# Kernel optimization log

Measured on AMD Instinct MI355X. Metric: run time of the kernel, lower is better.

The kernel has to match this reference:

```python
import jax, jax.numpy as jnp
import numpy as np


def setup_inputs() -> dict:
    key = jax.random.key(0)
    k1, k2 = jax.random.split(key)
    B, H, W, D = 4096, 64, 64, 512
    inputs = jax.random.normal(k1, (B, D), dtype=jnp.float32)
    # keras 'random_uniform' initializer default range [-0.05, 0.05]
    weights_map = jax.random.uniform(k2, (H, W, D), dtype=jnp.float32,
                                     minval=-0.05, maxval=0.05)
    return {"inputs": inputs, "weights_map": weights_map}


def reference(inputs, weights_map):
    # inputs: (B, D); weights_map: (H, W, D)
    H, W, D = weights_map.shape
    flat_w = weights_map.reshape(-1, D)              # (N, D), N = H*W
    # avoids materializing the (B, N, D) difference tensor)
    x_sq = jnp.sum(inputs * inputs, axis=1, keepdims=True)    # (B, 1)
    w_sq = jnp.sum(flat_w * flat_w, axis=1)                   # (N,)
    sq_dist = x_sq - 2.0 * (inputs @ flat_w.T) + w_sq         # (B, N)
    sq_dist = jnp.maximum(sq_dist, 0.0)
    bmu_flat = jnp.argmin(sq_dist, axis=1)                    # (B,)
    bmu_y = (bmu_flat // W).astype(jnp.int32)
    bmu_x = (bmu_flat % W).astype(jnp.int32)
    bmu_indices = jnp.stack([bmu_y, bmu_x], axis=1)           # (B, 2)
    min_sq = jnp.take_along_axis(sq_dist, bmu_flat[:, None], axis=1)[:, 0]
    quantization_errors = jnp.sqrt(min_sq)                    # (B,)
    return bmu_indices, quantization_errors
```

## Files before the change

kernel.cpp:

```cpp
#include <hip/hip_runtime.h>

#define B_ROWS 4096
#define N_COLS 4096
#define DIM    512
#define LDK    1024

typedef __attribute__((ext_vector_type(8))) short short8;
typedef __attribute__((ext_vector_type(4))) float floatx4;

__device__ __forceinline__ unsigned short f2bf_rn(float f) {
    unsigned u = __float_as_uint(f);
    u += 0x7fffu + ((u >> 16) & 1u);
    return (unsigned short)(u >> 16);
}
__device__ __forceinline__ float bf2f(unsigned short h) {
    return __uint_as_float(((unsigned)h) << 16);
}

__device__ __forceinline__ unsigned long long pack_key(float v, int idx) {
    unsigned u = __float_as_uint(v);
    u = (u & 0x80000000u) ? ~u : (u | 0x80000000u);
    return ((unsigned long long)u << 32) | (unsigned)idx;
}

__device__ __forceinline__ void async16(const unsigned short* g, unsigned short* l) {
    __builtin_amdgcn_global_load_lds(
        (__attribute__((address_space(1))) void*)g,
        (__attribute__((address_space(3))) void*)l, 16, 0, 0);
}

__global__ __launch_bounds__(256) void som_convert(
    const float* __restrict__ X, const float* __restrict__ Wt,
    unsigned short* __restrict__ Xc, unsigned short* __restrict__ Wc,
    float* __restrict__ x_sq, float* __restrict__ w_sq,
    unsigned long long* __restrict__ packed)
{
    int wave = threadIdx.x >> 6, lane = threadIdx.x & 63;
    int grow = blockIdx.x * 4 + wave;
    bool isX = grow < B_ROWS;
    const float* src = isX ? (X + (size_t)grow * DIM)
                           : (Wt + (size_t)(grow - B_ROWS) * DIM);
    const float4* p4 = (const float4*)src;
    float4 a = p4[lane * 2], b = p4[lane * 2 + 1];
    float f[8] = {a.x, a.y, a.z, a.w, b.x, b.y, b.z, b.w};
    short8 hi, lo;
    float s = 0.f;
    #pragma unroll
    for (int t = 0; t < 8; ++t) {
        unsigned short h = f2bf_rn(f[t]);
        hi[t] = (short)h;
        lo[t] = (short)f2bf_rn(f[t] - bf2f(h));
        s = fmaf(f[t], f[t], s);
    }
    unsigned short* dst = (isX ? Xc + (size_t)grow * LDK
                               : Wc + (size_t)(grow - B_ROWS) * LDK) + lane * 8;
    *(short8*)(dst)       = hi;
    *(short8*)(dst + 512) = lo;
    #pragma unroll
    for (int off = 32; off >= 1; off >>= 1) s += __shfl_xor(s, off, 64);
    if (lane == 0) {
        if (isX) { x_sq[grow] = s; packed[grow] = ~0ull; }
        else     { w_sq[grow - B_ROWS] = s; }
    }
}

#define MFMA16(AF, BF, I0)                                      \
    _Pragma("unroll")                                           \
    for (int i = 0; i < 4; ++i)                                 \
        _Pragma("unroll")                                       \
        for (int j = 0; j < 4; ++j)                             \
            acc[(I0) + i][j] = __builtin_amdgcn_mfma_f32_16x16x32_bf16( \
                AF[i], BF[j], acc[(I0) + i][j], 0, 0, 0);

#define PH_EXEC(MF)                                             \
    __builtin_amdgcn_s_barrier();                               \
    asm volatile("s_waitcnt lgkmcnt(0)");                       \
    __builtin_amdgcn_s_setprio(1);                              \
    MF                                                          \
    __builtin_amdgcn_s_setprio(0);                              \
    __builtin_amdgcn_s_barrier();

__global__ __launch_bounds__(512, 2) void som_dist_v11(
    const unsigned short* __restrict__ Xc, const unsigned short* __restrict__ Wc,
    const float* __restrict__ w_sq, unsigned long long* __restrict__ packed)
{
    __shared__ __align__(16) unsigned short L[65536];
    const int tid  = threadIdx.x;
    const int wave = tid >> 6, lane = tid & 63;
    const int quad = lane >> 4, t16 = lane & 15;
    const int wr = wave >> 2, wc = wave & 3;
    const int bm = blockIdx.y, bn = blockIdx.x;

    const int srow = lane >> 2;
    const int scol = ((((lane & 3) - ((lane >> 3) & 3)) & 3)) * 8;
    const unsigned short* gAq[4];
    const unsigned short* gBq[4];
    #pragma unroll
    for (int q = 0; q < 4; ++q) {
        const int s = wave * 4 + q, rsub = s >> 1, h = s & 1;
        gAq[q] = Xc + (size_t)(bm * 256 + rsub * 16 + srow) * LDK + h * 512 + scol;
        gBq[q] = Wc + (size_t)(bn * 256 + rsub * 16 + srow) * LDK + h * 512 + scol;
    }

    const int rdw8 = (4 * t16 + ((quad + ((t16 >> 1) & 3)) & 3)) * 8;

    floatx4 acc[8][4];
    #pragma unroll
    for (int i = 0; i < 8; ++i)
        #pragma unroll
        for (int j = 0; j < 4; ++j) acc[i][j] = (floatx4){0.f, 0.f, 0.f, 0.f};

    #pragma unroll
    for (int t = 0; t < 2; ++t) {
        const int k0 = t * 32;
        unsigned short* RB = &L[32768 + t * 16384];
        unsigned short* RA = &L[t * 16384];
        #pragma unroll
        for (int q = 0; q < 4; ++q) async16(gBq[q] + k0, RB + (wave * 4 + q) * 512);
        #pragma unroll
        for (int q = 0; q < 4; ++q) async16(gAq[q] + k0, RA + (wave * 4 + q) * 512);
    }

    #pragma unroll 1
    for (int kt = 0; kt < 16; ++kt) {
        const int slot = kt & 1;
        const bool st = (kt < 14);
        const int k2 = (kt + 2) * 32;

        if (kt == 15) asm volatile("s_waitcnt vmcnt(0)");
        else          asm volatile("s_waitcnt vmcnt(8)");
        __builtin_amdgcn_s_barrier();

        const unsigned short* pA = &L[slot * 16384 + wr * 8192 + rdw8];
        const unsigned short* pB = &L[32768 + slot * 16384 + wc * 4096 + rdw8];
        short8 ah0[4], ah1[4], al0[4], al1[4], bh[4], bl[4];

        #pragma unroll
        for (int i = 0; i < 4; ++i) ah0[i] = *(const short8*)(pA + i * 1024);
        #pragma unroll
        for (int j = 0; j < 4; ++j) bh[j]  = *(const short8*)(pB + j * 1024);
        PH_EXEC(MFMA16(ah0, bh, 0))

        #pragma unroll
        for (int j = 0; j < 4; ++j) bl[j] = *(const short8*)(pB + j * 1024 + 512);
        PH_EXEC(MFMA16(ah0, bl, 0))

        #pragma unroll
        for (int i = 0; i < 4; ++i) al0[i] = *(const short8*)(pA + i * 1024 + 512);
        if (st) {
            unsigned short* RB = &L[32768 + slot * 16384];
            #pragma unroll
            for (int q = 0; q < 4; ++q) async16(gBq[q] + k2, RB + (wave * 4 + q) * 512);
        }
        PH_EXEC(MFMA16(al0, bh, 0))

        #pragma unroll
        for (int i = 0; i < 4; ++i) ah1[i] = *(const short8*)(pA + (4 + i) * 1024);
        #pragma unroll
        for (int i = 0; i < 4; ++i) al1[i] = *(const short8*)(pA + (4 + i) * 1024 + 512);
        PH_EXEC(MFMA16(ah1, bh, 4))

        if (st) {
            unsigned short* RA = &L[slot * 16384];
            #pragma unroll
            for (int q = 0; q < 4; ++q) async16(gAq[q] + k2, RA + (wave * 4 + q) * 512);
        }
        PH_EXEC(MFMA16(ah1, bl, 4))

        __builtin_amdgcn_s_setprio(1);
        MFMA16(al1, bh, 4)
        __builtin_amdgcn_s_setprio(0);
    }

    const int col0 = bn * 256 + wc * 64 + t16;
    float wq[4];
    #pragma unroll
    for (int j = 0; j < 4; ++j) wq[j] = w_sq[col0 + j * 16];
    const int row_base = bm * 256 + wr * 128 + quad * 4;
    #pragma unroll
    for (int i = 0; i < 8; ++i) {
        #pragma unroll
        for (int r = 0; r < 4; ++r) {
            unsigned long long best = ~0ull;
            #pragma unroll
            for (int j = 0; j < 4; ++j) {
                float val = fmaf(-2.f, acc[i][j][r], wq[j]);
                unsigned long long key = pack_key(val, col0 + j * 16);
                best = (key < best) ? key : best;
            }
            #pragma unroll
            for (int m = 1; m <= 8; m <<= 1) {
                unsigned long long o = __shfl_xor(best, m, 64);
                best = (o < best) ? o : best;
            }
            if (t16 == 0)
                atomicMin(&packed[row_base + i * 16 + r], best);
        }
    }
}

__global__ __launch_bounds__(256) void som_finalize(
    const unsigned long long* __restrict__ packed,
    const float* __restrict__ x_sq, float* __restrict__ out)
{
    int b = blockIdx.x * 256 + threadIdx.x;
    unsigned long long p = packed[b];
    unsigned idx = (unsigned)(p & 0xffffffffull);
    unsigned key = (unsigned)(p >> 32);
    unsigned u = (key & 0x80000000u) ? (key & 0x7fffffffu) : ~key;
    float val = __uint_as_float(u);
    float sq = fmaxf(x_sq[b] + val, 0.f);
    out[2 * b]     = (float)(idx >> 6);
    out[2 * b + 1] = (float)(idx & 63);
    out[2 * B_ROWS + b] = sqrtf(sq);
}

extern "C" void kernel_launch(void* const* d_in, const int* in_sizes, int n_in,
                              void* d_out, int out_size, void* d_ws, size_t ws_size,
                              hipStream_t stream) {
    const float* X  = (const float*)d_in[0];
    const float* Wt = (const float*)d_in[1];
    float* out = (float*)d_out;

    unsigned long long* packed = (unsigned long long*)d_ws;
    float* x_sq = (float*)((char*)d_ws + (32 << 10));
    float* w_sq = (float*)((char*)d_ws + (48 << 10));
    unsigned short* Xc = (unsigned short*)((char*)d_ws + (64 << 10));
    unsigned short* Wc = (unsigned short*)((char*)d_ws + (64 << 10) + ((size_t)B_ROWS * LDK * 2));

    som_convert<<<dim3((B_ROWS + N_COLS) / 4), dim3(256), 0, stream>>>(
        X, Wt, Xc, Wc, x_sq, w_sq, packed);
    som_dist_v11<<<dim3(N_COLS / 256, B_ROWS / 256), dim3(512), 0, stream>>>(
        Xc, Wc, w_sq, packed);
    som_finalize<<<dim3(B_ROWS / 256), dim3(256), 0, stream>>>(packed, x_sq, out);
}
```

Baseline: 116.8 us.

## Load W fragments directly to registers from pre-swizzled layout, halve LDS

The convert kernel now writes the W matrix in a fragment-ordered layout, so each wave can load its MFMA B operands straight from global memory into registers and double-buffer them across k-steps. Only the X tile still goes through LDS, which halves shared-memory use and removes the B-side LDS reads and async copies. The block index is also remapped so that neighbouring blocks on the same XCD share W column tiles. The risks are extra register pressure from the b0/b1 buffers and global-load latency now sitting directly on the MFMA path.

```diff
diff --git a/kernel.cpp b/kernel.cpp
--- a/kernel.cpp
+++ b/kernel.cpp
@@ -38,8 +38,9 @@
     int wave = threadIdx.x >> 6, lane = threadIdx.x & 63;
     int grow = blockIdx.x * 4 + wave;
     bool isX = grow < B_ROWS;
-    const float* src = isX ? (X + (size_t)grow * DIM)
-                           : (Wt + (size_t)(grow - B_ROWS) * DIM);
+    int local = isX ? grow : grow - B_ROWS;
+    const float* src = isX ? (X + (size_t)local * DIM)
+                           : (Wt + (size_t)local * DIM);
     const float4* p4 = (const float4*)src;
     float4 a = p4[lane * 2], b = p4[lane * 2 + 1];
     float f[8] = {a.x, a.y, a.z, a.w, b.x, b.y, b.z, b.w};
@@ -52,15 +53,22 @@
         lo[t] = (short)f2bf_rn(f[t] - bf2f(h));
         s = fmaf(f[t], f[t], s);
     }
-    unsigned short* dst = (isX ? Xc + (size_t)grow * LDK
-                               : Wc + (size_t)(grow - B_ROWS) * LDK) + lane * 8;
-    *(short8*)(dst)       = hi;
-    *(short8*)(dst + 512) = lo;
-    #pragma unroll
-    for (int off = 32; off >= 1; off >>= 1) s += __shfl_xor(s, off, 64);
+    if (isX) {
+        unsigned short* dst = Xc + (size_t)local * LDK + lane * 8;
+        *(short8*)(dst)       = hi;
+        *(short8*)(dst + 512) = lo;
+    } else {
+        int R = local >> 4, rr = local & 15;
+        size_t off = ((size_t)R * 16 + (lane >> 2)) * 1024
+                   + (size_t)(rr + 16 * (lane & 3)) * 8;
+        *(short8*)(Wc + off)       = hi;
+        *(short8*)(Wc + off + 512) = lo;
+    }
+    #pragma unroll
+    for (int o = 32; o >= 1; o >>= 1) s += __shfl_xor(s, o, 64);
     if (lane == 0) {
         if (isX) { x_sq[grow] = s; packed[grow] = ~0ull; }
-        else     { w_sq[grow - B_ROWS] = s; }
+        else     { w_sq[local] = s; }
     }
 }
 
@@ -70,7 +78,7 @@
         _Pragma("unroll")                                       \
         for (int j = 0; j < 4; ++j)                             \
             acc[(I0) + i][j] = __builtin_amdgcn_mfma_f32_16x16x32_bf16( \
-                AF[i], BF[j], acc[(I0) + i][j], 0, 0, 0);
+                AF[i], (BF)[j], acc[(I0) + i][j], 0, 0, 0);
 
 #define PH_EXEC(MF)                                             \
     __builtin_amdgcn_s_barrier();                               \
@@ -80,29 +88,74 @@
     __builtin_amdgcn_s_setprio(0);                              \
     __builtin_amdgcn_s_barrier();
 
-__global__ __launch_bounds__(512, 2) void som_dist_v11(
+#define DIST_STEP(KT, SLOTBASE, BCUR, BNXT)                                    \
+{                                                                              \
+    if ((KT) == 15) asm volatile("s_waitcnt vmcnt(0)");                        \
+    else            asm volatile("s_waitcnt vmcnt(8)");                        \
+    __builtin_amdgcn_s_barrier();                                              \
+    if ((KT) < 15) {                                                           \
+        _Pragma("unroll")                                                      \
+        for (int j = 0; j < 4; ++j) {                                          \
+            BNXT[j]     = *(const short8*)(gBw + j * 16384 + ((KT) + 1) * 1024);       \
+            BNXT[4 + j] = *(const short8*)(gBw + j * 16384 + ((KT) + 1) * 1024 + 512); \
+        }                                                                      \
+    }                                                                          \
+    const unsigned short* pA = (SLOTBASE) + wr * 8192 + rdw8;                  \
+    short8 ah0[4], al0[4], ah1[4], al1[4];                                     \
+    _Pragma("unroll")                                                          \
+    for (int i = 0; i < 4; ++i) ah0[i] = *(const short8*)(pA + i * 1024);      \
+    PH_EXEC(MFMA16(ah0, BCUR, 0))                                              \
+    _Pragma("unroll")                                                          \
+    for (int i = 0; i < 4; ++i) al0[i] = *(const short8*)(pA + i * 1024 + 512);\
+    PH_EXEC(MFMA16(ah0, (&BCUR[4]), 0))                                        \
+    _Pragma("unroll")                                                          \
+    for (int i = 0; i < 4; ++i) ah1[i] = *(const short8*)(pA + (4+i) * 1024);  \
+    PH_EXEC(MFMA16(al0, BCUR, 0))                                              \
+    _Pragma("unroll")                                                          \
+    for (int i = 0; i < 4; ++i) al1[i] = *(const short8*)(pA + (4+i) * 1024 + 512); \
+    PH_EXEC(MFMA16(ah1, BCUR, 4))                                              \
+    if ((KT) < 14) {                                                           \
+        unsigned short* sd = (unsigned short*)(SLOTBASE);                      \
+        _Pragma("unroll")                                                      \
+        for (int q = 0; q < 4; ++q)                                            \
+            async16(gAq[q] + ((KT) + 2) * 32, sd + (wave * 4 + q) * 512);      \
+    }                                                                          \
+    __builtin_amdgcn_s_setprio(1);                                             \
+    MFMA16(ah1, (&BCUR[4]), 4)                                                 \
+    MFMA16(al1, BCUR, 4)                                                       \
+    __builtin_amdgcn_s_setprio(0);                                             \
+}
+
+__global__ __launch_bounds__(512, 2) void som_dist_v12(
     const unsigned short* __restrict__ Xc, const unsigned short* __restrict__ Wc,
     const float* __restrict__ w_sq, unsigned long long* __restrict__ packed)
 {
-    __shared__ __align__(16) unsigned short L[65536];
+    __shared__ __align__(16) unsigned short L[32768];
     const int tid  = threadIdx.x;
     const int wave = tid >> 6, lane = tid & 63;
     const int quad = lane >> 4, t16 = lane & 15;
     const int wr = wave >> 2, wc = wave & 3;
-    const int bm = blockIdx.y, bn = blockIdx.x;
+
+    const int bid = blockIdx.y * 16 + blockIdx.x;
+    const int xcd = bid & 7, wix = bid >> 3;
+    const int bn = xcd * 2 + (wix & 1);
+    const int bm = wix >> 1;
 
     const int srow = lane >> 2;
     const int scol = ((((lane & 3) - ((lane >> 3) & 3)) & 3)) * 8;
     const unsigned short* gAq[4];
-    const unsigned short* gBq[4];
     #pragma unroll
     for (int q = 0; q < 4; ++q) {
         const int s = wave * 4 + q, rsub = s >> 1, h = s & 1;
         gAq[q] = Xc + (size_t)(bm * 256 + rsub * 16 + srow) * LDK + h * 512 + scol;
-        gBq[q] = Wc + (size_t)(bn * 256 + rsub * 16 + srow) * LDK + h * 512 + scol;
-    }
+    }
+
+    const unsigned short* gBw = Wc + (size_t)(bn * 16 + wc * 4) * 16384 + lane * 8;
 
     const int rdw8 = (4 * t16 + ((quad + ((t16 >> 1) & 3)) & 3)) * 8;
+
+    unsigned short* const L0 = &L[0];
+    unsigned short* const L1 = &L[16384];
 
     floatx4 acc[8][4];
     #pragma unroll
@@ -110,66 +163,23 @@
         #pragma unroll
         for (int j = 0; j < 4; ++j) acc[i][j] = (floatx4){0.f, 0.f, 0.f, 0.f};
 
-    #pragma unroll
-    for (int t = 0; t < 2; ++t) {
-        const int k0 = t * 32;
-        unsigned short* RB = &L[32768 + t * 16384];
-        unsigned short* RA = &L[t * 16384];
-        #pragma unroll
-        for (int q = 0; q < 4; ++q) async16(gBq[q] + k0, RB + (wave * 4 + q) * 512);
-        #pragma unroll
-        for (int q = 0; q < 4; ++q) async16(gAq[q] + k0, RA + (wave * 4 + q) * 512);
-    }
+    short8 b0[8], b1[8];
+
+    #pragma unroll
+    for (int q = 0; q < 4; ++q) async16(gAq[q],      L0 + (wave * 4 + q) * 512);
+    #pragma unroll
+    for (int j = 0; j < 4; ++j) {
+        b0[j]     = *(const short8*)(gBw + j * 16384);
+        b0[4 + j] = *(const short8*)(gBw + j * 16384 + 512);
+    }
+    #pragma unroll
+    for (int q = 0; q < 4; ++q) async16(gAq[q] + 32, L1 + (wave * 4 + q) * 512);
 
     #pragma unroll 1
-    for (int kt = 0; kt < 16; ++kt) {
-        const int slot = kt & 1;
-        const bool st = (kt < 14);
-        const int k2 = (kt + 2) * 32;
-
-        if (kt == 15) asm volatile("s_waitcnt vmcnt(0)");
-        else          asm volatile("s_waitcnt vmcnt(8)");
-        __builtin_amdgcn_s_barrier();
-
-        const unsigned short* pA = &L[slot * 16384 + wr * 8192 + rdw8];
-        const unsigned short* pB = &L[32768 + slot * 16384 + wc * 4096 + rdw8];
-        short8 ah0[4], ah1[4], al0[4], al1[4], bh[4], bl[4];
-
-        #pragma unroll
-        for (int i = 0; i < 4; ++i) ah0[i] = *(const short8*)(pA + i * 1024);
-        #pragma unroll
-        for (int j = 0; j < 4; ++j) bh[j]  = *(const short8*)(pB + j * 1024);
-        PH_EXEC(MFMA16(ah0, bh, 0))
-
-        #pragma unroll
-        for (int j = 0; j < 4; ++j) bl[j] = *(const short8*)(pB + j * 1024 + 512);
-        PH_EXEC(MFMA16(ah0, bl, 0))
-
-        #pragma unroll
-        for (int i = 0; i < 4; ++i) al0[i] = *(const short8*)(pA + i * 1024 + 512);
-        if (st) {
-            unsigned short* RB = &L[32768 + slot * 16384];
-            #pragma unroll
-            for (int q = 0; q < 4; ++q) async16(gBq[q] + k2, RB + (wave * 4 + q) * 512);
-        }
-        PH_EXEC(MFMA16(al0, bh, 0))
-
-        #pragma unroll
-        for (int i = 0; i < 4; ++i) ah1[i] = *(const short8*)(pA + (4 + i) * 1024);
-        #pragma unroll
-        for (int i = 0; i < 4; ++i) al1[i] = *(const short8*)(pA + (4 + i) * 1024 + 512);
-        PH_EXEC(MFMA16(ah1, bh, 4))
-
-        if (st) {
-            unsigned short* RA = &L[slot * 16384];
-            #pragma unroll
-            for (int q = 0; q < 4; ++q) async16(gAq[q] + k2, RA + (wave * 4 + q) * 512);
-        }
-        PH_EXEC(MFMA16(ah1, bl, 4))
-
-        __builtin_amdgcn_s_setprio(1);
-        MFMA16(al1, bh, 4)
-        __builtin_amdgcn_s_setprio(0);
+    for (int k2 = 0; k2 < 8; ++k2) {
+        const int kt = k2 * 2;
+        DIST_STEP(kt,     L0, b0, b1)
+        DIST_STEP(kt + 1, L1, b1, b0)
     }
 
     const int col0 = bn * 256 + wc * 64 + t16;
@@ -230,7 +240,7 @@
 
     som_convert<<<dim3((B_ROWS + N_COLS) / 4), dim3(256), 0, stream>>>(
         X, Wt, Xc, Wc, x_sq, w_sq, packed);
-    som_dist_v11<<<dim3(N_COLS / 256, B_ROWS / 256), dim3(512), 0, stream>>>(
+    som_dist_v12<<<dim3(N_COLS / 256, B_ROWS / 256), dim3(512), 0, stream>>>(
         Xc, Wc, w_sq, packed);
     som_finalize<<<dim3(B_ROWS / 256), dim3(256), 0, stream>>>(packed, x_sq, out);
 }
```

Result: slower. 132.0 us (+13.0%).

## Restructure GEMM main loop with register-prefetched fragments and single barrier per step

Applied to the files above, without the earlier changes.

Replaces the per-phase barrier schedule (ten barriers per k-step) with one barrier per k-step. The first A/B fragments of the next LDS slot are prefetched into registers while the tail MFMAs of the current step run, with the loop unrolled by two to ping-pong register sets. Global async loads now wait with vmcnt(0) before the barrier, which may expose more global latency in exchange for less barrier stalling. Register pressure rises from holding two fragment sets.

```diff
diff --git a/kernel.cpp b/kernel.cpp
--- a/kernel.cpp
+++ b/kernel.cpp
@@ -72,15 +72,58 @@
             acc[(I0) + i][j] = __builtin_amdgcn_mfma_f32_16x16x32_bf16( \
                 AF[i], BF[j], acc[(I0) + i][j], 0, 0, 0);
 
-#define PH_EXEC(MF)                                             \
-    __builtin_amdgcn_s_barrier();                               \
-    asm volatile("s_waitcnt lgkmcnt(0)");                       \
-    __builtin_amdgcn_s_setprio(1);                              \
-    MF                                                          \
-    __builtin_amdgcn_s_setprio(0);                              \
-    __builtin_amdgcn_s_barrier();
-
-__global__ __launch_bounds__(512, 2) void som_dist_v11(
+#define DIST_STEP(KT, SCUR, SNXT, A0C, BHC, A0N, BHN)                          \
+{                                                                              \
+    const unsigned short* pA = &L[(SCUR) * 16384 + wr * 8192 + rdw8];          \
+    const unsigned short* pB = &L[32768 + (SCUR) * 16384 + wc * 4096 + rdw8];  \
+    short8 bl[4], al0[4], ah1[4], al1[4];                                      \
+           \
+    __builtin_amdgcn_s_setprio(1);                                             \
+    MFMA16(A0C, BHC, 0)                                                        \
+    __builtin_amdgcn_s_setprio(0);                                             \
+    _Pragma("unroll")                                                          \
+    for (int j = 0; j < 4; ++j) bl[j]  = *(const short8*)(pB + j * 1024 + 512);\
+    _Pragma("unroll")                                                          \
+    for (int i = 0; i < 4; ++i) al0[i] = *(const short8*)(pA + i * 1024 + 512);\
+    __builtin_amdgcn_s_setprio(1);                                             \
+    MFMA16(A0C, bl, 0)                                                         \
+    MFMA16(al0, BHC, 0)                                                        \
+    __builtin_amdgcn_s_setprio(0);                                             \
+    _Pragma("unroll")                                                          \
+    for (int i = 0; i < 4; ++i) ah1[i] = *(const short8*)(pA + (4 + i) * 1024);\
+    _Pragma("unroll")                                                          \
+    for (int i = 0; i < 4; ++i) al1[i] = *(const short8*)(pA + (4 + i) * 1024 + 512); \
+      \
+    asm volatile("s_waitcnt vmcnt(0)" ::: "memory");                           \
+    asm volatile("s_waitcnt lgkmcnt(0)" ::: "memory");                         \
+    __builtin_amdgcn_s_barrier();                                              \
+    asm volatile("" ::: "memory");                                             \
+    if ((KT) < 14) {                                                           \
+        unsigned short* RB = &L[32768 + (SCUR) * 16384];                       \
+        unsigned short* RA = &L[(SCUR) * 16384];                               \
+        const int k2o = ((KT) + 2) * 32;                                       \
+        _Pragma("unroll")                                                      \
+        for (int q = 0; q < 4; ++q) async16(gBq[q] + k2o, RB + (wave * 4 + q) * 512); \
+        _Pragma("unroll")                                                      \
+        for (int q = 0; q < 4; ++q) async16(gAq[q] + k2o, RA + (wave * 4 + q) * 512); \
+    }                                                                          \
+    if ((KT) < 15) {                                                           \
+        const unsigned short* qA = &L[(SNXT) * 16384 + wr * 8192 + rdw8];      \
+        const unsigned short* qB = &L[32768 + (SNXT) * 16384 + wc * 4096 + rdw8]; \
+        _Pragma("unroll")                                                      \
+        for (int i = 0; i < 4; ++i) A0N[i] = *(const short8*)(qA + i * 1024);  \
+        _Pragma("unroll")                                                      \
+        for (int j = 0; j < 4; ++j) BHN[j] = *(const short8*)(qB + j * 1024);  \
+    }                                                                          \
+                   \
+    __builtin_amdgcn_s_setprio(1);                                             \
+    MFMA16(ah1, BHC, 4)                                                        \
+    MFMA16(ah1, bl, 4)                                                         \
+    MFMA16(al1, BHC, 4)                                                        \
+    __builtin_amdgcn_s_setprio(0);                                             \
+}
+
+__global__ __launch_bounds__(512, 2) void som_dist_v14(
     const unsigned short* __restrict__ Xc, const unsigned short* __restrict__ Wc,
     const float* __restrict__ w_sq, unsigned long long* __restrict__ packed)
 {
@@ -120,56 +163,25 @@
         #pragma unroll
         for (int q = 0; q < 4; ++q) async16(gAq[q] + k0, RA + (wave * 4 + q) * 512);
     }
+    asm volatile("s_waitcnt vmcnt(8)" ::: "memory");
+    __builtin_amdgcn_s_barrier();
+    asm volatile("" ::: "memory");
+
+    short8 a0A[4], bhA[4], a0B[4], bhB[4];
+    {
+        const unsigned short* pA = &L[wr * 8192 + rdw8];
+        const unsigned short* pB = &L[32768 + wc * 4096 + rdw8];
+        #pragma unroll
+        for (int i = 0; i < 4; ++i) a0A[i] = *(const short8*)(pA + i * 1024);
+        #pragma unroll
+        for (int j = 0; j < 4; ++j) bhA[j] = *(const short8*)(pB + j * 1024);
+    }
 
     #pragma unroll 1
-    for (int kt = 0; kt < 16; ++kt) {
-        const int slot = kt & 1;
-        const bool st = (kt < 14);
-        const int k2 = (kt + 2) * 32;
-
-        if (kt == 15) asm volatile("s_waitcnt vmcnt(0)");
-        else          asm volatile("s_waitcnt vmcnt(8)");
-        __builtin_amdgcn_s_barrier();
-
-        const unsigned short* pA = &L[slot * 16384 + wr * 8192 + rdw8];
-        const unsigned short* pB = &L[32768 + slot * 16384 + wc * 4096 + rdw8];
-        short8 ah0[4], ah1[4], al0[4], al1[4], bh[4], bl[4];
-
-        #pragma unroll
-        for (int i = 0; i < 4; ++i) ah0[i] = *(const short8*)(pA + i * 1024);
-        #pragma unroll
-        for (int j = 0; j < 4; ++j) bh[j]  = *(const short8*)(pB + j * 1024);
-        PH_EXEC(MFMA16(ah0, bh, 0))
-
-        #pragma unroll
-        for (int j = 0; j < 4; ++j) bl[j] = *(const short8*)(pB + j * 1024 + 512);
-        PH_EXEC(MFMA16(ah0, bl, 0))
-
-        #pragma unroll
-        for (int i = 0; i < 4; ++i) al0[i] = *(const short8*)(pA + i * 1024 + 512);
-        if (st) {
-            unsigned short* RB = &L[32768 + slot * 16384];
-            #pragma unroll
-            for (int q = 0; q < 4; ++q) async16(gBq[q] + k2, RB + (wave * 4 + q) * 512);
-        }
-        PH_EXEC(MFMA16(al0, bh, 0))
-
-        #pragma unroll
-        for (int i = 0; i < 4; ++i) ah1[i] = *(const short8*)(pA + (4 + i) * 1024);
-        #pragma unroll
-        for (int i = 0; i < 4; ++i) al1[i] = *(const short8*)(pA + (4 + i) * 1024 + 512);
-        PH_EXEC(MFMA16(ah1, bh, 4))
-
-        if (st) {
-            unsigned short* RA = &L[slot * 16384];
-            #pragma unroll
-            for (int q = 0; q < 4; ++q) async16(gAq[q] + k2, RA + (wave * 4 + q) * 512);
-        }
-        PH_EXEC(MFMA16(ah1, bl, 4))
-
-        __builtin_amdgcn_s_setprio(1);
-        MFMA16(al1, bh, 4)
-        __builtin_amdgcn_s_setprio(0);
+    for (int k2 = 0; k2 < 8; ++k2) {
+        const int kt = k2 * 2;
+        DIST_STEP(kt,     0, 1, a0A, bhA, a0B, bhB)
+        DIST_STEP(kt + 1, 1, 0, a0B, bhB, a0A, bhA)
     }
 
     const int col0 = bn * 256 + wc * 64 + t16;
@@ -230,7 +242,7 @@
 
     som_convert<<<dim3((B_ROWS + N_COLS) / 4), dim3(256), 0, stream>>>(
         X, Wt, Xc, Wc, x_sq, w_sq, packed);
-    som_dist_v11<<<dim3(N_COLS / 256, B_ROWS / 256), dim3(512), 0, stream>>>(
+    som_dist_v14<<<dim3(N_COLS / 256, B_ROWS / 256), dim3(512), 0, stream>>>(
         Xc, Wc, w_sq, packed);
     som_finalize<<<dim3(B_ROWS / 256), dim3(256), 0, stream>>>(packed, x_sq, out);
 }
```

After: 129.2 us. 1.11x slower.
